# Kernel optimization log

Hardware: AMD Instinct MI355X
Metric: run time of the kernel (lower is better)

## Reference

```python
import jax, jax.numpy as jnp
import numpy as np

B, S, D_IN, D_OUT = 2, 2048, 4096, 4096


def setup_inputs() -> dict:
    key = jax.random.key(0)
    kx, kw, kb = jax.random.split(key, 3)
    x = jax.random.normal(kx, (B, S, D_IN), dtype=jnp.float32)
    weight = jax.random.normal(kw, (D_OUT, D_IN), dtype=jnp.float32)
    bias = jax.random.normal(kb, (D_OUT,), dtype=jnp.float32)
    return {"x": x, "weight": weight, "bias": bias}


def reference(x, weight, bias):
    # FdaBinary forward is simply sign(); linear with binarized weight.
    w_bin = jnp.sign(weight)  # [D_OUT, D_IN], values in {-1, 0, +1}
    # F.linear: x @ w.T + b
    out = jnp.einsum("bsd,od->bso", x, w_bin) + bias
    return out
```

## Files before the change

### kernel.cpp

```cpp
#include <hip/hip_runtime.h>
#include <hip/hip_bf16.h>
#include <stdint.h>
#include <stddef.h>

#define M_DIM 4096
#define N_DIM 4096
#define K_DIM 4096
#define BM 256
#define BN 256
#define BK 64
#define NKT (K_DIM / BK)
#define BKB (BK * 2)
#define RSTRIDE ((size_t)64 * K_DIM * 2)

typedef __bf16 bf16;
typedef __attribute__((ext_vector_type(4))) __bf16 bf16x4;
typedef __attribute__((ext_vector_type(8))) __bf16 bf16x8;
typedef __attribute__((ext_vector_type(4))) float f32x4;

__global__ __launch_bounds__(256) void prep_kernel(const float* __restrict__ x,
                                                   const float* __restrict__ w,
                                                   bf16* __restrict__ xb,
                                                   bf16* __restrict__ wb) {
    const int idx = blockIdx.x * 256 + threadIdx.x;
    float4 xv = ((const float4*)x)[idx];
    bf16x4 xo;
    xo[0] = (bf16)xv.x; xo[1] = (bf16)xv.y; xo[2] = (bf16)xv.z; xo[3] = (bf16)xv.w;
    ((bf16x4*)xb)[idx] = xo;

    float4 wv = ((const float4*)w)[idx];
    bf16x4 wo;
    wo[0] = (bf16)((wv.x > 0.f) ? 1.f : ((wv.x < 0.f) ? -1.f : 0.f));
    wo[1] = (bf16)((wv.y > 0.f) ? 1.f : ((wv.y < 0.f) ? -1.f : 0.f));
    wo[2] = (bf16)((wv.z > 0.f) ? 1.f : ((wv.z < 0.f) ? -1.f : 0.f));
    wo[3] = (bf16)((wv.w > 0.f) ? 1.f : ((wv.w < 0.f) ? -1.f : 0.f));
    ((bf16x4*)wb)[idx] = wo;
}

__device__ __forceinline__ void load_lds16(const void* g, void* l) {
    __builtin_amdgcn_global_load_lds(
        (const __attribute__((address_space(1))) void*)g,
        (__attribute__((address_space(3))) void*)l, 16, 0, 0);
}

__global__ __launch_bounds__(512, 2) void gemm_bin_kernel(const bf16* __restrict__ A,
                                                          const bf16* __restrict__ Bw,
                                                          const float* __restrict__ bias,
                                                          float* __restrict__ C) {
    __shared__ __align__(16) bf16 As[2][BM * BK];
    __shared__ __align__(16) bf16 Bs[2][BM * BK];

    const int tid  = threadIdx.x;
    const int lane = tid & 63;
    const int wave = tid >> 6;
    const int wm   = wave >> 2;
    const int wn   = wave & 3;

    const int tileM = blockIdx.y * BM;
    const int tileN = blockIdx.x * BN;

    const int rowInC = lane >> 3;
    const int q_src  = (lane & 7) ^ rowInC;
    const char* aSrc = (const char*)A  + ((size_t)(tileM + wave * 8 + rowInC) * K_DIM + q_src * 8) * 2;
    const char* bSrc = (const char*)Bw + ((size_t)(tileN + wave * 8 + rowInC) * K_DIM + q_src * 8) * 2;

#define STAGE_A(B_, R_, KOFF_) load_lds16(aSrc + (size_t)(R_) * RSTRIDE + (KOFF_), \
                                          &As[B_][((R_) * 64 + wave * 8) * BK])
#define STAGE_B(B_, R_, KOFF_) load_lds16(bSrc + (size_t)(R_) * RSTRIDE + (KOFF_), \
                                          &Bs[B_][((R_) * 64 + wave * 8) * BK])

    f32x4 acc[8][4];
#pragma unroll
    for (int i = 0; i < 8; ++i)
#pragma unroll
        for (int j = 0; j < 4; ++j)
            acc[i][j] = (f32x4){0.f, 0.f, 0.f, 0.f};

    bf16x8 bfr[4][2];

    const int l15 = lane & 15;
    const int qf  = lane >> 4;
    const int fragRowA = wm * 128 + l15;
    const int fragRowB = wn * 64 + l15;
    const int s0 = (0 + qf) ^ (l15 & 7);
    const int s1 = (4 + qf) ^ (l15 & 7);

#define READ_A(B_, P_) \
    _Pragma("unroll") \
    for (int ii = 0; ii < 2; ++ii) { \
        af[ii][0] = *(const bf16x8*)&As[B_][(fragRowA + (2 * (P_) + ii) * 16) * BK + s0 * 8]; \
        af[ii][1] = *(const bf16x8*)&As[B_][(fragRowA + (2 * (P_) + ii) * 16) * BK + s1 * 8]; \
    }

#define READ_B(B_) \
    _Pragma("unroll") \
    for (int j = 0; j < 4; ++j) { \
        bfr[j][0] = *(const bf16x8*)&Bs[B_][(fragRowB + j * 16) * BK + s0 * 8]; \
        bfr[j][1] = *(const bf16x8*)&Bs[B_][(fragRowB + j * 16) * BK + s1 * 8]; \
    }

#define MFMA16(P_) \
    _Pragma("unroll") \
    for (int ii = 0; ii < 2; ++ii) \
        _Pragma("unroll") \
        for (int j = 0; j < 4; ++j) { \
            acc[2 * (P_) + ii][j] = __builtin_amdgcn_mfma_f32_16x16x32_bf16(af[ii][0], bfr[j][0], acc[2 * (P_) + ii][j], 0, 0, 0); \
            acc[2 * (P_) + ii][j] = __builtin_amdgcn_mfma_f32_16x16x32_bf16(af[ii][1], bfr[j][1], acc[2 * (P_) + ii][j], 0, 0, 0); \
        }

#define PHASE(B_, P_, ISS0, ISS1, TAIL) do { \
        bf16x8 af[2][2]; \
        READ_A(B_, P_); \
        if ((P_) == 0) READ_B(B_); \
        ISS0; \
        ISS1; \
        __builtin_amdgcn_s_barrier(); \
        __builtin_amdgcn_s_setprio(1); \
        MFMA16(P_); \
        __builtin_amdgcn_s_setprio(0); \
        TAIL; \
        __builtin_amdgcn_s_barrier(); \
        __builtin_amdgcn_sched_barrier(0); \
    } while (0)

#define KTILE(B_, K1_, K2_) do { \
        PHASE(B_, 0, STAGE_A((B_) ^ 1, 1, K1_), STAGE_A((B_) ^ 1, 3, K1_), (void)0); \
        PHASE(B_, 1, STAGE_B(B_, 0, K2_),       STAGE_B(B_, 1, K2_),       (void)0); \
        PHASE(B_, 2, STAGE_B(B_, 2, K2_),       STAGE_B(B_, 3, K2_),       (void)0); \
        PHASE(B_, 3, STAGE_A(B_, 0, K2_),       STAGE_A(B_, 2, K2_), \
              asm volatile("s_waitcnt vmcnt(6)" ::: "memory")); \
    } while (0)

    STAGE_B(0, 0, 0);   STAGE_B(0, 1, 0);   STAGE_B(0, 2, 0);   STAGE_B(0, 3, 0);
    STAGE_A(0, 0, 0);   STAGE_A(0, 2, 0);   STAGE_A(0, 1, 0);   STAGE_A(0, 3, 0);
    STAGE_B(1, 0, BKB); STAGE_B(1, 1, BKB); STAGE_B(1, 2, BKB); STAGE_B(1, 3, BKB);
    STAGE_A(1, 0, BKB); STAGE_A(1, 2, BKB);
    asm volatile("s_waitcnt vmcnt(6)" ::: "memory");
    __builtin_amdgcn_s_barrier();
    __builtin_amdgcn_sched_barrier(0);

    for (int kt = 0; kt < NKT; kt += 2) {
        const int k1a = (kt + 1) * BKB;
        const int k2a = (kt + 2 < NKT) ? (kt + 2) * BKB : 0;
        KTILE(0, k1a, k2a);
        const int k2b = (kt + 3 < NKT) ? (kt + 3) * BKB : 0;
        KTILE(1, k2a, k2b);
    }

#pragma unroll
    for (int j = 0; j < 4; ++j) {
        const int col = tileN + wn * 64 + j * 16 + l15;
        const float bv = bias[col];
#pragma unroll
        for (int i = 0; i < 8; ++i) {
            const int row0 = tileM + wm * 128 + i * 16 + (qf << 2);
#pragma unroll
            for (int rr = 0; rr < 4; ++rr) {
                C[(size_t)(row0 + rr) * N_DIM + col] = acc[i][j][rr] + bv;
            }
        }
    }

#undef STAGE_A
#undef STAGE_B
#undef READ_A
#undef READ_B
#undef MFMA16
#undef PHASE
#undef KTILE
}

extern "C" void kernel_launch(void* const* d_in, const int* in_sizes, int n_in,
                              void* d_out, int out_size, void* d_ws, size_t ws_size,
                              hipStream_t stream) {
    const float* x    = (const float*)d_in[0];
    const float* w    = (const float*)d_in[1];
    const float* bias = (const float*)d_in[2];
    float* out        = (float*)d_out;

    const int nElem = M_DIM * K_DIM;
    bf16* xb = (bf16*)d_ws;
    bf16* wb = xb + (size_t)nElem;

    prep_kernel<<<nElem / 4 / 256, 256, 0, stream>>>(x, w, xb, wb);

    dim3 grid(N_DIM / BN, M_DIM / BM);
    gemm_bin_kernel<<<grid, 512, 0, stream>>>(xb, wb, bias, out);
}
```

Baseline: 282.9 us.

## Fuse bf16 conversion and weight sign into GEMM staging via registers

```diff
diff --git a/kernel.cpp b/kernel.cpp
--- a/kernel.cpp
+++ b/kernel.cpp
@@ -10,43 +10,17 @@
 #define BN 256
 #define BK 64
 #define NKT (K_DIM / BK)
-#define BKB (BK * 2)
-#define RSTRIDE ((size_t)64 * K_DIM * 2)
+
+static_assert(M_DIM % BM == 0 && N_DIM % BN == 0 && K_DIM % BK == 0, "tiling");
 
 typedef __bf16 bf16;
-typedef __attribute__((ext_vector_type(4))) __bf16 bf16x4;
 typedef __attribute__((ext_vector_type(8))) __bf16 bf16x8;
 typedef __attribute__((ext_vector_type(4))) float f32x4;
 
-__global__ __launch_bounds__(256) void prep_kernel(const float* __restrict__ x,
-                                                   const float* __restrict__ w,
-                                                   bf16* __restrict__ xb,
-                                                   bf16* __restrict__ wb) {
-    const int idx = blockIdx.x * 256 + threadIdx.x;
-    float4 xv = ((const float4*)x)[idx];
-    bf16x4 xo;
-    xo[0] = (bf16)xv.x; xo[1] = (bf16)xv.y; xo[2] = (bf16)xv.z; xo[3] = (bf16)xv.w;
-    ((bf16x4*)xb)[idx] = xo;
-
-    float4 wv = ((const float4*)w)[idx];
-    bf16x4 wo;
-    wo[0] = (bf16)((wv.x > 0.f) ? 1.f : ((wv.x < 0.f) ? -1.f : 0.f));
-    wo[1] = (bf16)((wv.y > 0.f) ? 1.f : ((wv.y < 0.f) ? -1.f : 0.f));
-    wo[2] = (bf16)((wv.z > 0.f) ? 1.f : ((wv.z < 0.f) ? -1.f : 0.f));
-    wo[3] = (bf16)((wv.w > 0.f) ? 1.f : ((wv.w < 0.f) ? -1.f : 0.f));
-    ((bf16x4*)wb)[idx] = wo;
-}
-
-__device__ __forceinline__ void load_lds16(const void* g, void* l) {
-    __builtin_amdgcn_global_load_lds(
-        (const __attribute__((address_space(1))) void*)g,
-        (__attribute__((address_space(3))) void*)l, 16, 0, 0);
-}
-
-__global__ __launch_bounds__(512, 2) void gemm_bin_kernel(const bf16* __restrict__ A,
-                                                          const bf16* __restrict__ Bw,
-                                                          const float* __restrict__ bias,
-                                                          float* __restrict__ C) {
+__global__ __launch_bounds__(512, 2) void gemm_bin_fused(const float* __restrict__ A,
+                                                         const float* __restrict__ W,
+                                                         const float* __restrict__ bias,
+                                                         float* __restrict__ C) {
     __shared__ __align__(16) bf16 As[2][BM * BK];
     __shared__ __align__(16) bf16 Bs[2][BM * BK];
 
@@ -59,15 +33,44 @@
     const int tileM = blockIdx.y * BM;
     const int tileN = blockIdx.x * BN;
 
-    const int rowInC = lane >> 3;
-    const int q_src  = (lane & 7) ^ rowInC;
-    const char* aSrc = (const char*)A  + ((size_t)(tileM + wave * 8 + rowInC) * K_DIM + q_src * 8) * 2;
-    const char* bSrc = (const char*)Bw + ((size_t)(tileN + wave * 8 + rowInC) * K_DIM + q_src * 8) * 2;
+    const int sRow  = tid >> 3;
+    const int sG    = tid & 7;
+    const int sSlot = sG ^ (sRow & 7);
+    const float* aBase = A + (size_t)(tileM + sRow) * K_DIM + sG * 8;
+    const float* wBase = W + (size_t)(tileN + sRow) * K_DIM + sG * 8;
+    const int ldsOff = sRow * BK + sSlot * 8;
 
-#define STAGE_A(B_, R_, KOFF_) load_lds16(aSrc + (size_t)(R_) * RSTRIDE + (KOFF_), \
-                                          &As[B_][((R_) * 64 + wave * 8) * BK])
-#define STAGE_B(B_, R_, KOFF_) load_lds16(bSrc + (size_t)(R_) * RSTRIDE + (KOFF_), \
-                                          &Bs[B_][((R_) * 64 + wave * 8) * BK])
+#define ISSUE(DST_, BASE_, KB_) \
+    _Pragma("unroll") \
+    for (int r = 0; r < 4; ++r) { \
+        DST_[2 * r]     = *(const f32x4*)(BASE_ + (size_t)r * 64 * K_DIM + (KB_)); \
+        DST_[2 * r + 1] = *(const f32x4*)(BASE_ + (size_t)r * 64 * K_DIM + (KB_) + 4); \
+    }
+
+#define CVTWR_A(BUF_, SRC_) \
+    _Pragma("unroll") \
+    for (int r = 0; r < 4; ++r) { \
+        bf16x8 v; \
+        _Pragma("unroll") \
+        for (int e = 0; e < 4; ++e) { \
+            v[e]     = (bf16)SRC_[2 * r][e]; \
+            v[4 + e] = (bf16)SRC_[2 * r + 1][e]; \
+        } \
+        *(bf16x8*)&As[BUF_][r * 64 * BK + ldsOff] = v; \
+    }
+
+#define SGN(F_) ((bf16)(((F_) > 0.f) ? 1.f : (((F_) < 0.f) ? -1.f : 0.f)))
+#define CVTWR_B(BUF_, SRC_) \
+    _Pragma("unroll") \
+    for (int r = 0; r < 4; ++r) { \
+        bf16x8 v; \
+        _Pragma("unroll") \
+        for (int e = 0; e < 4; ++e) { \
+            v[e]     = SGN(SRC_[2 * r][e]); \
+            v[4 + e] = SGN(SRC_[2 * r + 1][e]); \
+        } \
+        *(bf16x8*)&Bs[BUF_][r * 64 * BK + ldsOff] = v; \
+    }
 
     f32x4 acc[8][4];
 #pragma unroll
@@ -108,43 +111,49 @@
             acc[2 * (P_) + ii][j] = __builtin_amdgcn_mfma_f32_16x16x32_bf16(af[ii][1], bfr[j][1], acc[2 * (P_) + ii][j], 0, 0, 0); \
         }
 
-#define PHASE(B_, P_, ISS0, ISS1, TAIL) do { \
-        bf16x8 af[2][2]; \
-        READ_A(B_, P_); \
-        if ((P_) == 0) READ_B(B_); \
-        ISS0; \
-        ISS1; \
-        __builtin_amdgcn_s_barrier(); \
-        __builtin_amdgcn_s_setprio(1); \
-        MFMA16(P_); \
-        __builtin_amdgcn_s_setprio(0); \
-        TAIL; \
-        __builtin_amdgcn_s_barrier(); \
-        __builtin_amdgcn_sched_barrier(0); \
+#define VMCNT0 asm volatile("s_waitcnt vmcnt(0)" ::: "memory")
+#define LGKM0  asm volatile("s_waitcnt lgkmcnt(0)" ::: "memory")
+#define BAR    __builtin_amdgcn_s_barrier()
+#define SCHED0 __builtin_amdgcn_sched_barrier(0)
+#define PRIO1  __builtin_amdgcn_s_setprio(1)
+#define PRIO0  __builtin_amdgcn_s_setprio(0)
+
+#define KTILE(B_, KN_) do { \
+        { bf16x8 af[2][2]; \
+          READ_B(B_); READ_A(B_, 0); \
+          BAR; PRIO1; MFMA16(0); PRIO0; BAR; SCHED0; } \
+        { bf16x8 af[2][2]; \
+          READ_A(B_, 1); \
+          ISSUE(aLd, aBase, KN_); \
+          BAR; PRIO1; MFMA16(1); PRIO0; BAR; SCHED0; } \
+        { bf16x8 af[2][2]; \
+          READ_A(B_, 2); \
+          VMCNT0; CVTWR_A((B_) ^ 1, aLd); SCHED0; \
+          ISSUE(bLd, wBase, KN_); \
+          BAR; PRIO1; MFMA16(2); PRIO0; BAR; SCHED0; } \
+        { bf16x8 af[2][2]; \
+          READ_A(B_, 3); \
+          VMCNT0; CVTWR_B((B_) ^ 1, bLd); LGKM0; \
+          BAR; PRIO1; MFMA16(3); PRIO0; BAR; SCHED0; } \
     } while (0)
 
-#define KTILE(B_, K1_, K2_) do { \
-        PHASE(B_, 0, STAGE_A((B_) ^ 1, 1, K1_), STAGE_A((B_) ^ 1, 3, K1_), (void)0); \
-        PHASE(B_, 1, STAGE_B(B_, 0, K2_),       STAGE_B(B_, 1, K2_),       (void)0); \
-        PHASE(B_, 2, STAGE_B(B_, 2, K2_),       STAGE_B(B_, 3, K2_),       (void)0); \
-        PHASE(B_, 3, STAGE_A(B_, 0, K2_),       STAGE_A(B_, 2, K2_), \
-              asm volatile("s_waitcnt vmcnt(6)" ::: "memory")); \
-    } while (0)
+    f32x4 aLd[8];
+    f32x4 bLd[8];
 
-    STAGE_B(0, 0, 0);   STAGE_B(0, 1, 0);   STAGE_B(0, 2, 0);   STAGE_B(0, 3, 0);
-    STAGE_A(0, 0, 0);   STAGE_A(0, 2, 0);   STAGE_A(0, 1, 0);   STAGE_A(0, 3, 0);
-    STAGE_B(1, 0, BKB); STAGE_B(1, 1, BKB); STAGE_B(1, 2, BKB); STAGE_B(1, 3, BKB);
-    STAGE_A(1, 0, BKB); STAGE_A(1, 2, BKB);
-    asm volatile("s_waitcnt vmcnt(6)" ::: "memory");
-    __builtin_amdgcn_s_barrier();
-    __builtin_amdgcn_sched_barrier(0);
+    ISSUE(aLd, aBase, 0);
+    ISSUE(bLd, wBase, 0);
+    VMCNT0;
+    CVTWR_A(0, aLd);
+    CVTWR_B(0, bLd);
+    LGKM0;
+    BAR;
+    SCHED0;
 
     for (int kt = 0; kt < NKT; kt += 2) {
-        const int k1a = (kt + 1) * BKB;
-        const int k2a = (kt + 2 < NKT) ? (kt + 2) * BKB : 0;
-        KTILE(0, k1a, k2a);
-        const int k2b = (kt + 3 < NKT) ? (kt + 3) * BKB : 0;
-        KTILE(1, k2a, k2b);
+        const int kn1 = (kt + 1 < NKT) ? (kt + 1) * BK : 0;
+        KTILE(0, kn1);
+        const int kn2 = (kt + 2 < NKT) ? (kt + 2) * BK : 0;
+        KTILE(1, kn2);
     }
 
 #pragma unroll
@@ -161,12 +170,19 @@
         }
     }
 
-#undef STAGE_A
-#undef STAGE_B
+#undef ISSUE
+#undef CVTWR_A
+#undef CVTWR_B
+#undef SGN
 #undef READ_A
 #undef READ_B
 #undef MFMA16
-#undef PHASE
+#undef VMCNT0
+#undef LGKM0
+#undef BAR
+#undef SCHED0
+#undef PRIO1
+#undef PRIO0
 #undef KTILE
 }
 
@@ -178,12 +194,6 @@
     const float* bias = (const float*)d_in[2];
     float* out        = (float*)d_out;
 
-    const int nElem = M_DIM * K_DIM;
-    bf16* xb = (bf16*)d_ws;
-    bf16* wb = xb + (size_t)nElem;
-
-    prep_kernel<<<nElem / 4 / 256, 256, 0, stream>>>(x, w, xb, wb);
-
     dim3 grid(N_DIM / BN, M_DIM / BM);
-    gemm_bin_kernel<<<grid, 512, 0, stream>>>(xb, wb, bias, out);
+    gemm_bin_fused<<<grid, 512, 0, stream>>>(x, w, bias, out);
 }
```

New measurement: 407.1 us. +43.9%, slower.
